# Performance work log

Hardware: AMD Instinct MI355X
Metric: run time of the kernel (lower is better)

The kernel has to match this reference:

```python
import jax, jax.numpy as jnp
import numpy as np

LRELU_ALPHA = 0.2       # LeakyReLU slope (alpha arg of GraphAttentionLayer)
NEG_INF = -9e15         # zero_vec value from the torch code
N1, N2, N3 = 3000, 2500, 2500
IN_F, OUT_F, HEADS = 128, 64, 2


def setup_inputs() -> dict:
    key = jax.random.key(0)
    ks = jax.random.split(key, 13)
    N = N1 + N2 + N3
    h = jax.random.normal(ks[0], (N, IN_F), jnp.float32)
    A1  = jax.random.randint(ks[1],  (N1, N1), 0, 2, jnp.int32)
    A2  = jax.random.randint(ks[2],  (N2, N2), 0, 2, jnp.int32)
    A3  = jax.random.randint(ks[3],  (N3, N3), 0, 2, jnp.int32)
    A12 = jax.random.randint(ks[4],  (N1, N2), 0, 2, jnp.int32)
    A13 = jax.random.randint(ks[5],  (N1, N3), 0, 2, jnp.int32)
    A23 = jax.random.randint(ks[6],  (N2, N3), 0, 2, jnp.int32)
    A21 = jax.random.randint(ks[7],  (N2, N1), 0, 2, jnp.int32)
    A31 = jax.random.randint(ks[8],  (N3, N1), 0, 2, jnp.int32)
    A32 = jax.random.randint(ks[9],  (N3, N2), 0, 2, jnp.int32)
    # per-head GAT parameters (xavier-ish scale)
    Ws = jax.random.normal(ks[10], (HEADS, IN_F, OUT_F), jnp.float32) * 0.12
    a_param = jax.random.normal(ks[11], (HEADS, 2 * OUT_F, 1), jnp.float32) * 0.12
    return dict(h=h, A1=A1, A2=A2, A3=A3, A12=A12, A13=A13, A23=A23,
                A21=A21, A31=A31, A32=A32, Ws=Ws, a_param=a_param)


def reference(h, A1, A2, A3, A12, A13, A23, A21, A31, A32, Ws, a_param):
    n1, n2, n3 = A1.shape[0], A2.shape[0], A3.shape[0]
    # The 9 block assignments in the torch forward tile the full NxN matrix,
    # so they are equivalent to one block-structured mask.
    mask = jnp.block([[A1,  A12, A13],
                      [A21, A2,  A23],
                      [A31, A32, A3]]) > 0          # [N, N] bool

    Wh = jnp.einsum('nf,hfo->hno', h, Ws)           # [H, N, O]
    a1 = a_param[:, :OUT_F, 0]                      # [H, O]
    a2 = a_param[:, OUT_F:, 0]                      # [H, O]
    Wh1 = jnp.einsum('hno,ho->hn', Wh, a1)          # [H, N]
    Wh2 = jnp.einsum('hno,ho->hn', Wh, a2)          # [H, N]
    e = jax.nn.leaky_relu(Wh1[:, :, None] + Wh2[:, None, :], LRELU_ALPHA)  # [H,N,N]
    att = jax.nn.softmax(jnp.where(mask[None], e, NEG_INF), axis=-1)
    # dropout is identity in eval mode
    mid = jnp.einsum('hij,hjo->hio', att, Wh)       # [H, N, O]
    out = jax.nn.elu(mid)                           # concat=True -> elu
    x2 = out.transpose(1, 0, 2).reshape(h.shape[0], -1)  # [N, H*O] head concat

    x3 = jax.nn.log_softmax(x2[n1 + n2:], axis=1)   # group-3 nodes
    x4 = jax.nn.log_softmax(x2[:n1], axis=1)        # group-1 nodes
    x5 = jax.nn.log_softmax(x2[n1:n1 + n2], axis=1) # group-2 nodes
    return (x3, x4, x5)
```

## Files before the change

kernel.cpp:

```cpp
#include <hip/hip_runtime.h>
#include <hip/hip_bf16.h>


#define CN1 3000
#define CN2 2500
#define CN3 2500
#define NTOT 8000
#define INF_ 128
#define OUTF 64
#define LOG2E 1.44269504088896340736f
#define ALPHA 0.2f

typedef __attribute__((ext_vector_type(4))) float f32x4;
typedef __attribute__((ext_vector_type(8))) short short8;
typedef __attribute__((ext_vector_type(4))) int i32x4;
union B16x8 { int4 i4; short8 s8; unsigned int u[4]; };

#if defined(__has_builtin)
#if __has_builtin(__builtin_amdgcn_exp2f)
#define EXP2F(x) __builtin_amdgcn_exp2f(x)
#endif
#endif
#ifndef EXP2F
#define EXP2F(x) exp2f(x)
#endif

__device__ inline float wave_sum(float v) {
  for (int d = 32; d; d >>= 1) v += __shfl_xor(v, d, 64);
  return v;
}

__device__ inline unsigned int pk2(float a, float b) {
  union { __hip_bfloat162 h; unsigned int u; } cv;
  cv.h = __float22bfloat162_rn(make_float2(a, b));
  return cv.u;
}

__device__ inline unsigned int pack2_bf16(float a, float b) {
  unsigned ua = __float_as_uint(a);
  ua = (ua + 0x7FFFu + ((ua >> 16) & 1u)) >> 16;
  unsigned ub = __float_as_uint(b);
  ub = (ub + 0x7FFFu + ((ub >> 16) & 1u)) & 0xFFFF0000u;
  return ub | ua;
}

__global__ __launch_bounds__(256)
void k_front(const int* __restrict__ A1,  const int* __restrict__ A12, const int* __restrict__ A13,
             const int* __restrict__ A21, const int* __restrict__ A2,  const int* __restrict__ A23,
             const int* __restrict__ A31, const int* __restrict__ A32, const int* __restrict__ A3,
             unsigned int* __restrict__ packed,
             const float* __restrict__ hv, const float* __restrict__ Wsv,
             const float* __restrict__ ap,
             float* __restrict__ Whf,
             float* __restrict__ Wh1s,
             float* __restrict__ Wh2s,
             unsigned int* __restrict__ E2pk) {
  if ((blockIdx.x & 1) == 0) {
    const int i = (blockIdx.x >> 1) * 4 + (threadIdx.x >> 6);
    const int lane = threadIdx.x & 63;
    const int *r0, *r1, *r2;
    if (i < CN1)            { r0 = A1  + i * CN1;          r1 = A12 + i * CN2;          r2 = A13 + i * CN3; }
    else if (i < CN1 + CN2) { int r = i - CN1;       r0 = A21 + r * CN1; r1 = A2  + r * CN2; r2 = A23 + r * CN3; }
    else                    { int r = i - CN1 - CN2; r0 = A31 + r * CN1; r1 = A32 + r * CN2; r2 = A3  + r * CN3; }
    const i32x4* p0 = (const i32x4*)r0;
    const i32x4* p1 = (const i32x4*)r1;
    const i32x4* p2 = (const i32x4*)r2;
    unsigned int* pkrow = packed + (i >> 4) * 4000 + (i & 15);
    const int sh = 4 * (lane & 7);
    const int w  = lane >> 3;
#pragma unroll
    for (int ob = 0; ob < 2; ++ob) {
      i32x4 v[16];
#pragma unroll
      for (int u = 0; u < 16; ++u) {
        int q = (ob * 16 + u) * 64 + lane;
        q = q < 2000 ? q : 1999;
        const i32x4* src = (q < 750) ? (p0 + q) : (q < 1375) ? (p1 + q - 750) : (p2 + q - 1375);
        v[u] = __builtin_nontemporal_load(src);
      }
#pragma unroll
      for (int u = 0; u < 16; ++u) {
        const int it = ob * 16 + u;
        const bool act = (it * 64 + lane) < 2000;
        unsigned int n = (v[u].x > 0 ? 1u : 0u) | (v[u].y > 0 ? 2u : 0u)
                       | (v[u].z > 0 ? 4u : 0u) | (v[u].w > 0 ? 8u : 0u);
        n = act ? (n << sh) : 0u;
        n |= __shfl_xor(n, 1, 64);
        n |= __shfl_xor(n, 2, 64);
        n |= __shfl_xor(n, 4, 64);
        const int wglob = it * 8 + w;
        if ((lane & 7) == 0 && wglob < 250)
          pkrow[wglob * 16] = n;
      }
    }
  } else {
    const int t = threadIdx.x;
    const int o = t & 63;
    const int n = (blockIdx.x >> 1) * 4 + (t >> 6);
    const float* hrow = hv + n * INF_;
    const float* Ws0 = Wsv + o;
    const float* Ws1 = Wsv + INF_ * OUTF + o;
    float a0a = 0.f, a0b = 0.f, a1a = 0.f, a1b = 0.f;
#pragma unroll 8
    for (int f = 0; f < INF_; f += 2) {
      float h0 = hrow[f], h1 = hrow[f + 1];
      a0a += h0 * Ws0[f * OUTF];
      a0b += h1 * Ws0[(f + 1) * OUTF];
      a1a += h0 * Ws1[f * OUTF];
      a1b += h1 * Ws1[(f + 1) * OUTF];
    }
    float acc0 = a0a + a0b, acc1 = a1a + a1b;
    Whf[(0 * NTOT + n) * OUTF + o] = acc0;
    Whf[(1 * NTOT + n) * OUTF + o] = acc1;
    float s10 = wave_sum(acc0 * ap[o]);
    float s20 = wave_sum(acc0 * ap[OUTF + o]);
    float s11 = wave_sum(acc1 * ap[2 * OUTF + o]);
    float s21 = wave_sum(acc1 * ap[3 * OUTF + o]);
    if (o == 0) {
      const float w20 = s20 * LOG2E, w21 = s21 * LOG2E;
      Wh1s[n] = s10 * LOG2E;        Wh2s[n] = w20;
      Wh1s[NTOT + n] = s11 * LOG2E; Wh2s[NTOT + n] = w21;
      E2pk[n]        = pk2(EXP2F(w20), EXP2F(ALPHA * w20));
      E2pk[NTOT + n] = pk2(EXP2F(w21), EXP2F(ALPHA * w21));
    }
  }
}

__global__ __launch_bounds__(256)
void k_mid(const float* __restrict__ Whf, const float* __restrict__ Wh2s,
           float* __restrict__ M2s, int4* __restrict__ WhB) {
  if (blockIdx.x < 2) {
    const int hd = blockIdx.x;
    float mx = -1e30f;
    for (int i = threadIdx.x; i < NTOT; i += 256)
      mx = fmaxf(mx, Wh2s[hd * NTOT + i]);
    for (int d = 32; d; d >>= 1) mx = fmaxf(mx, __shfl_xor(mx, d, 64));
    __shared__ float red[4];
    if ((threadIdx.x & 63) == 0) red[threadIdx.x >> 6] = mx;
    __syncthreads();
    if (threadIdx.x == 0)
      M2s[hd] = fmaxf(fmaxf(red[0], red[1]), fmaxf(red[2], red[3]));
  } else {
    const int gid = (blockIdx.x - 2) * 256 + threadIdx.x;
    const int lane = gid & 63;
    const int c = (gid >> 6) & 3;
    const int t = (gid >> 8) % 250;
    const int hd = gid / 64000;
    const int jb = t * 32 + (lane >> 4) * 8;
    const int col = c * 16 + (lane & 15);
    const float* src = Whf + (hd * NTOT + jb) * OUTF + col;
    B16x8 out;
#pragma unroll
    for (int e2 = 0; e2 < 4; ++e2)
      out.u[e2] = pack2_bf16(src[(2 * e2) * OUTF], src[(2 * e2 + 1) * OUTF]);
    WhB[gid] = out.i4;
  }
}

__global__ __launch_bounds__(128)
void k_attn_mfma(const unsigned int* __restrict__ packed,
                 const float* __restrict__ Wh1s,
                 const float* __restrict__ M2s, const int4* __restrict__ WhB,
                 const unsigned int* __restrict__ E2pk,
                 float* __restrict__ partAcc,
                 float* __restrict__ partS)
{
  const int hd = threadIdx.x >> 6;
  const int lane = threadIdx.x & 63;
  const int m = lane & 15;
  const int g = lane >> 4;
  const int kb = g * 8;
  const int rowblk = blockIdx.x;
  const int i = rowblk * 16 + m;
  const int jy = blockIdx.y, njy = gridDim.y;
  const int t0 = (250 * jy) / njy, t1 = (250 * (jy + 1)) / njy;

  const unsigned int* pkb = packed + rowblk * 4000 + m;

  const float w1s = Wh1s[hd * NTOT + i];
  const float y = w1s + M2s[hd];
  const float ci = fmaxf(y, ALPHA * y);
  const float E1p = EXP2F(w1s - ci);
  const float E1n = EXP2F(fmaf(ALPHA, w1s, -ci));
  const unsigned int* e2 = E2pk + hd * NTOT;
  const int4* WhBh = WhB + hd * 64000;

  f32x4 a_0 = {0.f,0.f,0.f,0.f}, a_1 = a_0, a_2 = a_0, a_3 = a_0;
  f32x4 sv = a_0;

  B16x8 ones;
#pragma unroll
  for (int e2i = 0; e2i < 4; ++e2i) ones.u[e2i] = 0x3F803F80u;

  struct Frags { int4 f[4]; uint4 ua, ub; };
  auto load_frags = [&](int t, Frags& F) {
    const int4* bp = WhBh + t * 256 + lane;
#pragma unroll
    for (int c = 0; c < 4; ++c) F.f[c] = bp[c * 64];
    const unsigned int* w0 = e2 + t * 32 + kb;
    F.ua = *(const uint4*)w0; F.ub = *(const uint4*)(w0 + 4);
  };

  auto compute = [&](unsigned int mw, const Frags& F) {
    const unsigned bits = (mw >> kb) & 0xffu;
    const unsigned uv[8] = {F.ua.x, F.ua.y, F.ua.z, F.ua.w, F.ub.x, F.ub.y, F.ub.z, F.ub.w};
    float q[8];
#pragma unroll
    for (int e = 0; e < 8; ++e) {
      bool on = ((bits >> e) & 1u) != 0u;
      float p = __uint_as_float(uv[e] << 16);
      float nn = __uint_as_float(uv[e] & 0xFFFF0000u);
      float v = fmaxf(E1p * p, E1n * nn);
      q[e] = on ? v : 0.f;
    }
    B16x8 af;
#pragma unroll
    for (int e2i = 0; e2i < 4; ++e2i)
      af.u[e2i] = pk2(q[2 * e2i], q[2 * e2i + 1]);
    B16x8 b;
    b.i4 = F.f[0]; a_0 = __builtin_amdgcn_mfma_f32_16x16x32_bf16(af.s8, b.s8, a_0, 0, 0, 0);
    b.i4 = F.f[1]; a_1 = __builtin_amdgcn_mfma_f32_16x16x32_bf16(af.s8, b.s8, a_1, 0, 0, 0);
    b.i4 = F.f[2]; a_2 = __builtin_amdgcn_mfma_f32_16x16x32_bf16(af.s8, b.s8, a_2, 0, 0, 0);
    b.i4 = F.f[3]; a_3 = __builtin_amdgcn_mfma_f32_16x16x32_bf16(af.s8, b.s8, a_3, 0, 0, 0);
    sv = __builtin_amdgcn_mfma_f32_16x16x32_bf16(af.s8, ones.s8, sv, 0, 0, 0);
  };

  unsigned int mw0 = pkb[t0 * 16];
  unsigned int mw1 = pkb[min(t0 + 1, t1 - 1) * 16];
  Frags FA, FB;
  load_frags(t0, FA);
  int t = t0;
  for (; t + 1 < t1; t += 2) {
    load_frags(t + 1, FB);
    unsigned int mwa = pkb[min(t + 2, t1 - 1) * 16];
    compute(mw0, FA);
    mw0 = mw1; mw1 = mwa;
    load_frags(min(t + 2, t1 - 1), FA);
    unsigned int mwb = pkb[min(t + 3, t1 - 1) * 16];
    compute(mw0, FB);
    mw0 = mw1; mw1 = mwb;
  }
  if (t < t1) compute(mw0, FA);

  const int base = (jy * 2 + hd) * NTOT + rowblk * 16;
  if (m == 0) {
#pragma unroll
    for (int q = 0; q < 4; ++q)
      partS[base + g * 4 + q] = sv[q];
  }
  float* o = partAcc + base * OUTF;
#pragma unroll
  for (int q = 0; q < 4; ++q) {
    const int row = g * 4 + q;
    o[row * OUTF +      m] = a_0[q];
    o[row * OUTF + 16 + m] = a_1[q];
    o[row * OUTF + 32 + m] = a_2[q];
    o[row * OUTF + 48 + m] = a_3[q];
  }
}

__global__ void k_final(const float* __restrict__ partAcc, const float* __restrict__ partS,
                        int njy, float* __restrict__ out) {
  const int wave = threadIdx.x >> 6, lane = threadIdx.x & 63;
  const int n = blockIdx.x * 4 + wave;
  float x[2];
#pragma unroll
  for (int hd = 0; hd < 2; ++hd) {
    float a = 0.f, s = 0.f;
    for (int jy = 0; jy < njy; ++jy) {
      a += partAcc[((jy * 2 + hd) * NTOT + n) * OUTF + lane];
      s += partS[(jy * 2 + hd) * NTOT + n];
    }
    float mid = a / s;
    x[hd] = mid > 0.f ? mid : (__expf(mid) - 1.f);
  }
  float mx = fmaxf(x[0], x[1]);
  for (int d = 32; d; d >>= 1) mx = fmaxf(mx, __shfl_xor(mx, d, 64));
  float se = __expf(x[0] - mx) + __expf(x[1] - mx);
  for (int d = 32; d; d >>= 1) se += __shfl_xor(se, d, 64);
  const float lse = mx + __logf(se);
  const int orow = (n >= CN1 + CN2) ? (n - CN1 - CN2) : (n + CN3);
  out[orow * 128 + lane]      = x[0] - lse;
  out[orow * 128 + 64 + lane] = x[1] - lse;
}

__global__ void k_sentinel(float* __restrict__ out, float v) {
  out[blockIdx.x * 256 + threadIdx.x] = v;
}

extern "C" void kernel_launch(void* const* d_in, const int* in_sizes, int n_in,
                              void* d_out, int out_size, void* d_ws, size_t ws_size,
                              hipStream_t stream) {
  float* outf = (float*)d_out;

  static const int EXP[12] = {1024000, 9000000, 6250000, 6250000, 7500000, 7500000,
                              6250000, 7500000, 7500000, 6250000, 16384, 256};
  bool exact = (n_in == 12);
  if (exact) for (int i = 0; i < 12; ++i) if (in_sizes[i] != EXP[i]) { exact = false; break; }

  const size_t FIXED = 64000 + 64000 + 256 + 64000 + 2048000 + 8000000;
  int njy = 0;
  for (int cand = 8; cand >= 1; cand >>= 1) {
    size_t need = FIXED + (size_t)cand * 64000 + (size_t)cand * 4096000;
    if (ws_size >= need) { njy = cand; break; }
  }
  if (!exact || njy == 0) {
    k_sentinel<<<dim3(4000), dim3(256), 0, stream>>>(outf, -148.0f);
    return;
  }

  const float* h  = (const float*)d_in[0];
  const int* A1  = (const int*)d_in[1];
  const int* A2  = (const int*)d_in[2];
  const int* A3  = (const int*)d_in[3];
  const int* A12 = (const int*)d_in[4];
  const int* A13 = (const int*)d_in[5];
  const int* A23 = (const int*)d_in[6];
  const int* A21 = (const int*)d_in[7];
  const int* A31 = (const int*)d_in[8];
  const int* A32 = (const int*)d_in[9];
  const float* Ws = (const float*)d_in[10];
  const float* ap = (const float*)d_in[11];

  char* w = (char*)d_ws;
  float*        Wh1s    = (float*)(w);
  float*        Wh2s    = (float*)(w + 64000);
  float*        M2s     = (float*)(w + 128000);
  unsigned int* E2pk    = (unsigned int*)(w + 128256);
  int4*         WhB     = (int4*) (w + 192256);
  unsigned int* packed  = (unsigned int*)(w + 2240256);
  float*        partS   = (float*)(w + 10240256);
  float*        Whf     = (float*)(w + 10240256 + (size_t)njy * 64000);
  float*        partAcc = Whf;

  k_front    <<<dim3(4000),     dim3(256), 0, stream>>>(A1, A12, A13, A21, A2, A23, A31, A32, A3,
                                                        packed, h, Ws, ap, Whf, Wh1s, Wh2s, E2pk);
  k_mid      <<<dim3(502),      dim3(256), 0, stream>>>(Whf, Wh2s, M2s, WhB);
  k_attn_mfma<<<dim3(500, njy), dim3(128), 0, stream>>>(packed, Wh1s, M2s, WhB, E2pk,
                                                        partAcc, partS);
  k_final    <<<dim3(2000),     dim3(256), 0, stream>>>(partAcc, partS, njy, outf);
}
```

Before: 329.7 us.

## Process two 16-row blocks per attention wave to reuse Wh fragments

Each wave in the attention kernel now handles two 16-row blocks instead of one, so every B-fragment of Wh and every packed E2 value it loads feeds MFMAs for both row blocks. This halves global/L2 traffic for Wh fragments per output row, and the grid x-dimension is halved to match. The cost is roughly double the accumulator registers, which may lower occupancy, and fewer blocks overall to spread across CUs.

```diff
diff --git a/kernel.cpp b/kernel.cpp
--- a/kernel.cpp
+++ b/kernel.cpp
@@ -170,23 +170,28 @@
   const int m = lane & 15;
   const int g = lane >> 4;
   const int kb = g * 8;
-  const int rowblk = blockIdx.x;
-  const int i = rowblk * 16 + m;
+  const int rbA = blockIdx.x * 2;
+  const int rbB = rbA + 1;
+  const int iA = rbA * 16 + m;
+  const int iB = rbB * 16 + m;
   const int jy = blockIdx.y, njy = gridDim.y;
   const int t0 = (250 * jy) / njy, t1 = (250 * (jy + 1)) / njy;
 
-  const unsigned int* pkb = packed + rowblk * 4000 + m;
-
-  const float w1s = Wh1s[hd * NTOT + i];
-  const float y = w1s + M2s[hd];
-  const float ci = fmaxf(y, ALPHA * y);
-  const float E1p = EXP2F(w1s - ci);
-  const float E1n = EXP2F(fmaf(ALPHA, w1s, -ci));
+  const unsigned int* pkbA = packed + rbA * 4000 + m;
+  const unsigned int* pkbB = packed + rbB * 4000 + m;
+
+  const float w1sA = Wh1s[hd * NTOT + iA];
+  const float w1sB = Wh1s[hd * NTOT + iB];
+  const float yA = w1sA + M2s[hd], yB = w1sB + M2s[hd];
+  const float ciA = fmaxf(yA, ALPHA * yA), ciB = fmaxf(yB, ALPHA * yB);
+  const float E1pA = EXP2F(w1sA - ciA), E1nA = EXP2F(fmaf(ALPHA, w1sA, -ciA));
+  const float E1pB = EXP2F(w1sB - ciB), E1nB = EXP2F(fmaf(ALPHA, w1sB, -ciB));
   const unsigned int* e2 = E2pk + hd * NTOT;
   const int4* WhBh = WhB + hd * 64000;
 
-  f32x4 a_0 = {0.f,0.f,0.f,0.f}, a_1 = a_0, a_2 = a_0, a_3 = a_0;
-  f32x4 sv = a_0;
+  f32x4 aA_0 = {0.f,0.f,0.f,0.f}, aA_1 = aA_0, aA_2 = aA_0, aA_3 = aA_0;
+  f32x4 aB_0 = aA_0, aB_1 = aA_0, aB_2 = aA_0, aB_3 = aA_0;
+  f32x4 svA = aA_0, svB = aA_0;
 
   B16x8 ones;
 #pragma unroll
@@ -201,61 +206,84 @@
     F.ua = *(const uint4*)w0; F.ub = *(const uint4*)(w0 + 4);
   };
 
-  auto compute = [&](unsigned int mw, const Frags& F) {
-    const unsigned bits = (mw >> kb) & 0xffu;
+  auto compute = [&](unsigned int mwA, unsigned int mwB, const Frags& F) {
+    const unsigned bitsA = (mwA >> kb) & 0xffu;
+    const unsigned bitsB = (mwB >> kb) & 0xffu;
     const unsigned uv[8] = {F.ua.x, F.ua.y, F.ua.z, F.ua.w, F.ub.x, F.ub.y, F.ub.z, F.ub.w};
-    float q[8];
+    float qA[8], qB[8];
 #pragma unroll
     for (int e = 0; e < 8; ++e) {
-      bool on = ((bits >> e) & 1u) != 0u;
       float p = __uint_as_float(uv[e] << 16);
       float nn = __uint_as_float(uv[e] & 0xFFFF0000u);
-      float v = fmaxf(E1p * p, E1n * nn);
-      q[e] = on ? v : 0.f;
-    }
-    B16x8 af;
-#pragma unroll
-    for (int e2i = 0; e2i < 4; ++e2i)
-      af.u[e2i] = pk2(q[2 * e2i], q[2 * e2i + 1]);
+      float vA = fmaxf(E1pA * p, E1nA * nn);
+      float vB = fmaxf(E1pB * p, E1nB * nn);
+      qA[e] = ((bitsA >> e) & 1u) ? vA : 0.f;
+      qB[e] = ((bitsB >> e) & 1u) ? vB : 0.f;
+    }
+    B16x8 afA, afB;
+#pragma unroll
+    for (int e2i = 0; e2i < 4; ++e2i) {
+      afA.u[e2i] = pk2(qA[2 * e2i], qA[2 * e2i + 1]);
+      afB.u[e2i] = pk2(qB[2 * e2i], qB[2 * e2i + 1]);
+    }
     B16x8 b;
-    b.i4 = F.f[0]; a_0 = __builtin_amdgcn_mfma_f32_16x16x32_bf16(af.s8, b.s8, a_0, 0, 0, 0);
-    b.i4 = F.f[1]; a_1 = __builtin_amdgcn_mfma_f32_16x16x32_bf16(af.s8, b.s8, a_1, 0, 0, 0);
-    b.i4 = F.f[2]; a_2 = __builtin_amdgcn_mfma_f32_16x16x32_bf16(af.s8, b.s8, a_2, 0, 0, 0);
-    b.i4 = F.f[3]; a_3 = __builtin_amdgcn_mfma_f32_16x16x32_bf16(af.s8, b.s8, a_3, 0, 0, 0);
-    sv = __builtin_amdgcn_mfma_f32_16x16x32_bf16(af.s8, ones.s8, sv, 0, 0, 0);
+    b.i4 = F.f[0];
+    aA_0 = __builtin_amdgcn_mfma_f32_16x16x32_bf16(afA.s8, b.s8, aA_0, 0, 0, 0);
+    aB_0 = __builtin_amdgcn_mfma_f32_16x16x32_bf16(afB.s8, b.s8, aB_0, 0, 0, 0);
+    b.i4 = F.f[1];
+    aA_1 = __builtin_amdgcn_mfma_f32_16x16x32_bf16(afA.s8, b.s8, aA_1, 0, 0, 0);
+    aB_1 = __builtin_amdgcn_mfma_f32_16x16x32_bf16(afB.s8, b.s8, aB_1, 0, 0, 0);
+    b.i4 = F.f[2];
+    aA_2 = __builtin_amdgcn_mfma_f32_16x16x32_bf16(afA.s8, b.s8, aA_2, 0, 0, 0);
+    aB_2 = __builtin_amdgcn_mfma_f32_16x16x32_bf16(afB.s8, b.s8, aB_2, 0, 0, 0);
+    b.i4 = F.f[3];
+    aA_3 = __builtin_amdgcn_mfma_f32_16x16x32_bf16(afA.s8, b.s8, aA_3, 0, 0, 0);
+    aB_3 = __builtin_amdgcn_mfma_f32_16x16x32_bf16(afB.s8, b.s8, aB_3, 0, 0, 0);
+    svA = __builtin_amdgcn_mfma_f32_16x16x32_bf16(afA.s8, ones.s8, svA, 0, 0, 0);
+    svB = __builtin_amdgcn_mfma_f32_16x16x32_bf16(afB.s8, ones.s8, svB, 0, 0, 0);
   };
 
-  unsigned int mw0 = pkb[t0 * 16];
-  unsigned int mw1 = pkb[min(t0 + 1, t1 - 1) * 16];
+  unsigned int mwA0 = pkbA[t0 * 16],                 mwB0 = pkbB[t0 * 16];
+  unsigned int mwA1 = pkbA[min(t0 + 1, t1 - 1) * 16], mwB1 = pkbB[min(t0 + 1, t1 - 1) * 16];
   Frags FA, FB;
   load_frags(t0, FA);
   int t = t0;
   for (; t + 1 < t1; t += 2) {
     load_frags(t + 1, FB);
-    unsigned int mwa = pkb[min(t + 2, t1 - 1) * 16];
-    compute(mw0, FA);
-    mw0 = mw1; mw1 = mwa;
-    load_frags(min(t + 2, t1 - 1), FA);
-    unsigned int mwb = pkb[min(t + 3, t1 - 1) * 16];
-    compute(mw0, FB);
-    mw0 = mw1; mw1 = mwb;
-  }
-  if (t < t1) compute(mw0, FA);
-
-  const int base = (jy * 2 + hd) * NTOT + rowblk * 16;
+    const int tna = min(t + 2, t1 - 1);
+    unsigned int mwAa = pkbA[tna * 16], mwBa = pkbB[tna * 16];
+    compute(mwA0, mwB0, FA);
+    mwA0 = mwA1; mwB0 = mwB1; mwA1 = mwAa; mwB1 = mwBa;
+    load_frags(tna, FA);
+    const int tnb = min(t + 3, t1 - 1);
+    unsigned int mwAb = pkbA[tnb * 16], mwBb = pkbB[tnb * 16];
+    compute(mwA0, mwB0, FB);
+    mwA0 = mwA1; mwB0 = mwB1; mwA1 = mwAb; mwB1 = mwBb;
+  }
+  if (t < t1) compute(mwA0, mwB0, FA);
+
+  const int baseA = (jy * 2 + hd) * NTOT + rbA * 16;
+  const int baseB = (jy * 2 + hd) * NTOT + rbB * 16;
   if (m == 0) {
 #pragma unroll
-    for (int q = 0; q < 4; ++q)
-      partS[base + g * 4 + q] = sv[q];
-  }
-  float* o = partAcc + base * OUTF;
+    for (int q = 0; q < 4; ++q) {
+      partS[baseA + g * 4 + q] = svA[q];
+      partS[baseB + g * 4 + q] = svB[q];
+    }
+  }
+  float* oA = partAcc + baseA * OUTF;
+  float* oB = partAcc + baseB * OUTF;
 #pragma unroll
   for (int q = 0; q < 4; ++q) {
     const int row = g * 4 + q;
-    o[row * OUTF +      m] = a_0[q];
-    o[row * OUTF + 16 + m] = a_1[q];
-    o[row * OUTF + 32 + m] = a_2[q];
-    o[row * OUTF + 48 + m] = a_3[q];
+    oA[row * OUTF +      m] = aA_0[q];
+    oA[row * OUTF + 16 + m] = aA_1[q];
+    oA[row * OUTF + 32 + m] = aA_2[q];
+    oA[row * OUTF + 48 + m] = aA_3[q];
+    oB[row * OUTF +      m] = aB_0[q];
+    oB[row * OUTF + 16 + m] = aB_1[q];
+    oB[row * OUTF + 32 + m] = aB_2[q];
+    oB[row * OUTF + 48 + m] = aB_3[q];
   }
 }
 
@@ -336,7 +364,7 @@
   k_front    <<<dim3(4000),     dim3(256), 0, stream>>>(A1, A12, A13, A21, A2, A23, A31, A32, A3,
                                                         packed, h, Ws, ap, Whf, Wh1s, Wh2s, E2pk);
   k_mid      <<<dim3(502),      dim3(256), 0, stream>>>(Whf, Wh2s, M2s, WhB);
-  k_attn_mfma<<<dim3(500, njy), dim3(128), 0, stream>>>(packed, Wh1s, M2s, WhB, E2pk,
+  k_attn_mfma<<<dim3(250, njy), dim3(128), 0, stream>>>(packed, Wh1s, M2s, WhB, E2pk,
                                                         partAcc, partS);
   k_final    <<<dim3(2000),     dim3(256), 0, stream>>>(partAcc, partS, njy, outf);
 }
```

Measured after the change: 329.5 us. Within noise of the previous version (-0.1%).
